# Performance work log

Measured on AMD Instinct MI355X. Metric: run time of the kernel, lower is better.

The kernel has to match this reference:

```python
import math
import jax, jax.numpy as jnp
import numpy as np

KV_RANK = 512
NOPE = 128
ROPE = 64
V_DIM = 128
N_HEADS = 16
DIM = 2048
EPS = 1e-6
# qk_head_dim = 192; max_seq_len > original_seq_len -> mscale correction
_MSCALE = 0.1 * 1.0 * math.log(40.0) + 1.0
SOFTMAX_SCALE = (NOPE + ROPE) ** -0.5 * _MSCALE * _MSCALE


def _rmsnorm(x, w):
    y = x * jax.lax.rsqrt(jnp.mean(x * x, axis=-1, keepdims=True) + EPS)
    return y * w


def _rope(x, cos, sin):
    # x: [b, s, h, d] with d even; pairs are interleaved (complex view semantics)
    xr, xi = x[..., 0::2], x[..., 1::2]
    c = cos[None, :, None, :]
    s = sin[None, :, None, :]
    yr = xr * c - xi * s
    yi = xr * s + xi * c
    return jnp.stack([yr, yi], axis=-1).reshape(x.shape)


def setup_inputs() -> dict:
    key = jax.random.key(0)
    ks = jax.random.split(key, 6)
    B, S = 2, 2048
    x = jax.random.normal(ks[0], (B, S, DIM), dtype=jnp.float32)
    # standard RoPE angles: pos * inv_freq, theta=10000
    inv_freq = 1.0 / (10000.0 ** (np.arange(0, ROPE, 2, dtype=np.float32) / ROPE))
    angles = jnp.asarray(np.arange(S, dtype=np.float32)[:, None] * inv_freq[None, :])
    wq = jax.random.normal(ks[1], (N_HEADS * (NOPE + ROPE), DIM), dtype=jnp.float32) * (DIM ** -0.5)
    wkv_a = jax.random.normal(ks[2], (KV_RANK + ROPE, DIM), dtype=jnp.float32) * (DIM ** -0.5)
    wkv_b = jax.random.normal(ks[3], (N_HEADS * (NOPE + V_DIM), KV_RANK), dtype=jnp.float32) * (KV_RANK ** -0.5)
    wo = jax.random.normal(ks[4], (DIM, N_HEADS * V_DIM), dtype=jnp.float32) * ((N_HEADS * V_DIM) ** -0.5)
    kv_norm_w = jnp.ones((KV_RANK,), dtype=jnp.float32)
    return {"x": x, "angles": angles, "wq": wq, "wkv_a": wkv_a,
            "wkv_b": wkv_b, "wo": wo, "kv_norm_w": kv_norm_w}


def reference(x, angles, wq, wkv_a, wkv_b, wo, kv_norm_w):
    B, S, _ = x.shape
    cos, sin = jnp.cos(angles), jnp.sin(angles)  # [S, ROPE//2]

    # query projection
    q = (x @ wq.T).reshape(B, S, N_HEADS, NOPE + ROPE)
    q_nope, q_pe = q[..., :NOPE], q[..., NOPE:]
    q_pe = _rope(q_pe, cos, sin)

    # low-rank kv projection
    kv = x @ wkv_a.T  # [B, S, KV_RANK + ROPE]
    kv_c, k_pe = kv[..., :KV_RANK], kv[..., KV_RANK:]
    k_pe = _rope(k_pe[:, :, None, :], cos, sin)[:, :, 0]  # [B, S, ROPE]
    c = _rmsnorm(kv_c, kv_norm_w)  # latent kv cache [B, S, KV_RANK]

    # weight absorption: fold W^UK into q
    wkv_b_h = wkv_b.reshape(N_HEADS, NOPE + V_DIM, KV_RANK)
    q_abs = jnp.einsum('bshd,hdc->bshc', q_nope, wkv_b_h[:, :NOPE])

    scores = (jnp.einsum('bshc,btc->bsht', q_abs, c)
              + jnp.einsum('bshr,btr->bsht', q_pe, k_pe)) * SOFTMAX_SCALE

    # causal mask (prefill, start_pos=0)
    mask = jnp.where(jnp.tril(jnp.ones((S, S), dtype=bool)), 0.0, -jnp.inf)
    scores = scores + mask[None, :, None, :]
    probs = jax.nn.softmax(scores.astype(jnp.float32), axis=-1).astype(x.dtype)

    o_lat = jnp.einsum('bsht,btc->bshc', probs, c)
    o = jnp.einsum('bshc,hdc->bshd', o_lat, wkv_b_h[:, NOPE:])  # [B,S,H,V]
    return o.reshape(B, S, N_HEADS * V_DIM) @ wo.T
```

## Files before the change

### kernel.cpp

```cpp
#include <hip/hip_runtime.h>
#include <hip/hip_bf16.h>

typedef unsigned short u16;
typedef unsigned int   u32;
typedef __attribute__((ext_vector_type(8))) short bf16x8;
typedef __attribute__((ext_vector_type(4))) float f32x4;

#define NH   16
#define SS   2048

__device__ __forceinline__ u16 bf16b(float f) {
  union { float f; u32 u; } v; v.f = f;
  u32 r = (v.u + 0x7fffu + ((v.u >> 16) & 1u)) >> 16;
  return (u16)r;
}
__device__ __forceinline__ float bf2f(u16 v) {
  union { u32 u; float f; } x; x.u = (u32)v << 16; return x.f;
}
__device__ __forceinline__ f32x4 mfma16(bf16x8 a, bf16x8 b, f32x4 c) {
  return __builtin_amdgcn_mfma_f32_16x16x32_bf16(a, b, c, 0, 0, 0);
}
__device__ __forceinline__ void gl_lds16(const u16* g, u16* l) {
  __builtin_amdgcn_global_load_lds(
      (const __attribute__((address_space(1))) void*)g,
      (__attribute__((address_space(3))) void*)l, 16, 0, 0);
}

__global__ __launch_bounds__(256) void zerok(float* __restrict__ p, long n)
{
  long i = ((long)blockIdx.x * 256 + threadIdx.x) * 4;
  if (i < n) { p[i] = 0.f; p[i+1] = 0.f; p[i+2] = 0.f; p[i+3] = 0.f; }
}

__global__ __launch_bounds__(256) void castk(const float* __restrict__ src,
                                             u16* __restrict__ dst, long n)
{
  long i = ((long)blockIdx.x * 256 + threadIdx.x) * 4;
  if (i >= n) return;
  const float4 f = *(const float4*)(src + i);
  uint2 v;
  v.x = (u32)bf16b(f.x) | ((u32)bf16b(f.y) << 16);
  v.y = (u32)bf16b(f.z) | ((u32)bf16b(f.w) << 16);
  *(uint2*)(dst + i) = v;
}

__global__ __launch_bounds__(256) void wsplit(const float* __restrict__ wb,
                                              u16* __restrict__ T1, u16* __restrict__ Wv)
{
  const long i = (long)blockIdx.x * 256 + threadIdx.x;
  const int h   = (int)(i >> 16);
  const int rem = (int)(i & 65535);
  { const int c = rem >> 7, d = rem & 127;
    T1[i] = bf16b(wb[((long)(h * 256 + d)) * 512 + c]); }
  { const int d = rem >> 9, c = rem & 511;
    Wv[i] = bf16b(wb[((long)(h * 256 + 128 + d)) * 512 + c]); }
}

template<int OUTBF>
__global__ __launch_bounds__(256, 2)
void gemm_bt(const u16* __restrict__ A, const u16* __restrict__ W, void* __restrict__ Cout,
             int M, int N, int K, int lda, int ldw, int ldc,
             long aStride, long wStride, long cStride)
{
  __shared__ u16 As[128 * 40];
  __shared__ u16 Bs[128 * 40];
  const int tid = threadIdx.x;
  const int wave = tid >> 6, lane = tid & 63, g = lane >> 4, l15 = lane & 15;
  const int z = blockIdx.z;
  A += (long)z * aStride;  W += (long)z * wStride;
  const long cOff = (long)z * cStride;
  const int m0 = blockIdx.y * 128, n0 = blockIdx.x * 128;
  const int mq = (wave >> 1) * 64, nq = (wave & 1) * 64;
  const int srow = tid >> 1, scol = (tid & 1) * 16;

  const f32x4 fzero = {0.f, 0.f, 0.f, 0.f};
  f32x4 acc[4][4];
#pragma unroll
  for (int i = 0; i < 4; i++)
#pragma unroll
    for (int j = 0; j < 4; j++) acc[i][j] = fzero;

  for (int k0 = 0; k0 < K; k0 += 32) {
    const u16* aSrc = A + (long)(m0 + srow) * lda + k0 + scol;
    uint4 av0 = *(const uint4*)aSrc;
    uint4 av1 = *(const uint4*)(aSrc + 8);
    uint4 bv0 = make_uint4(0, 0, 0, 0), bv1 = make_uint4(0, 0, 0, 0);
    if (n0 + srow < N) {
      const u16* wSrc = W + (long)(n0 + srow) * ldw + k0 + scol;
      bv0 = *(const uint4*)wSrc;
      bv1 = *(const uint4*)(wSrc + 8);
    }
    __syncthreads();
    *(uint4*)&As[srow * 40 + scol]     = av0;
    *(uint4*)&As[srow * 40 + scol + 8] = av1;
    *(uint4*)&Bs[srow * 40 + scol]     = bv0;
    *(uint4*)&Bs[srow * 40 + scol + 8] = bv1;
    __syncthreads();

    bf16x8 af[4], bfr[4];
#pragma unroll
    for (int i = 0; i < 4; i++) af[i]  = *(const bf16x8*)&As[(mq + i * 16 + l15) * 40 + g * 8];
#pragma unroll
    for (int j = 0; j < 4; j++) bfr[j] = *(const bf16x8*)&Bs[(nq + j * 16 + l15) * 40 + g * 8];
#pragma unroll
    for (int i = 0; i < 4; i++)
#pragma unroll
      for (int j = 0; j < 4; j++)
        acc[i][j] = mfma16(af[i], bfr[j], acc[i][j]);
  }

#pragma unroll
  for (int i = 0; i < 4; i++) {
    const int r0 = m0 + mq + i * 16 + g * 4;
#pragma unroll
    for (int j = 0; j < 4; j++) {
      const int c = n0 + nq + j * 16 + l15;
      if (c < N) {
#pragma unroll
        for (int r = 0; r < 4; r++) {
          const long idx = cOff + (long)(r0 + r) * ldc + c;
          if (OUTBF) ((u16*)Cout)[idx]   = bf16b(acc[i][j][r]);
          else       ((float*)Cout)[idx] = acc[i][j][r];
        }
      }
    }
  }
}

__global__ __launch_bounds__(256) void qpack(const u16* __restrict__ q,
                                             const float* __restrict__ angles,
                                             u16* __restrict__ qpe)
{
  const int s = blockIdx.x;
  const int sseq = s & (SS - 1);
  const int tid = threadIdx.x;
#pragma unroll
  for (int pp = 0; pp < 2; pp++) {
    const int p = tid * 2 + pp;
    const int h = p >> 5, j = p & 31;
    const float xr = bf2f(q[(long)s * 3072 + h * 192 + 128 + 2 * j]);
    const float xi = bf2f(q[(long)s * 3072 + h * 192 + 128 + 2 * j + 1]);
    float sn, cs;
    __sincosf(angles[sseq * 32 + j], &sn, &cs);
    const u32 pk = (u32)bf16b(xr * cs - xi * sn) | ((u32)bf16b(xr * sn + xi * cs) << 16);
    *(u32*)(qpe + ((long)s * NH + h) * 64 + 2 * j) = pk;
  }
}

__global__ __launch_bounds__(256) void kvpack(const u16* __restrict__ kv,
                                              const float* __restrict__ angles,
                                              const float* __restrict__ kvw,
                                              u16* __restrict__ cb, u16* __restrict__ kpe)
{
  const int row = blockIdx.x * 4 + (threadIdx.x >> 6);
  const int lane = threadIdx.x & 63;
  const int sseq = row & (SS - 1);
  const u16* src = kv + (long)row * 576;
  float v[8]; float ss = 0.f;
#pragma unroll
  for (int j = 0; j < 8; j++) { float t = bf2f(src[lane + j * 64]); v[j] = t; ss += t * t; }
#pragma unroll
  for (int d = 1; d < 64; d <<= 1) ss += __shfl_xor(ss, d, 64);
  const float rn = 1.0f / sqrtf(ss * (1.f / 512.f) + 1e-6f);
#pragma unroll
  for (int j = 0; j < 8; j++)
    cb[(long)row * 512 + lane + j * 64] = bf16b(v[j] * rn * kvw[lane + j * 64]);
  if (lane < 32) {
    const float xr = bf2f(src[512 + 2 * lane]), xi = bf2f(src[512 + 2 * lane + 1]);
    float sn, cs;
    __sincosf(angles[sseq * 32 + lane], &sn, &cs);
    const u32 pk = (u32)bf16b(xr * cs - xi * sn) | ((u32)bf16b(xr * sn + xi * cs) << 16);
    *(u32*)(kpe + (long)row * 64 + 2 * lane) = pk;
  }
}

__global__ __launch_bounds__(256, 2)
void attn_flash(const u16* __restrict__ qab, const u16* __restrict__ qpe,
                const u16* __restrict__ cb, const u16* __restrict__ kpe,
                u16* __restrict__ olat)
{
  __shared__ u16 KsD[2][16 * 512];
  __shared__ u16 KrD[2][16 * 64];
  __shared__ u16 VT[512 * 32];
  __shared__ u16 Ps[4][16 * 40];

  const int tid = threadIdx.x;
  const int wave = tid >> 6, lane = tid & 63;
  const int g = lane >> 4, l15 = lane & 15;
  const int bh = blockIdx.y, b = bh >> 4, h = bh & 15;
  const int bx = blockIdx.x;
  const int s0 = bx * 64;
  const int swave = s0 + wave * 16;
  const float NEG_INF = -__builtin_inff();
  const float SC = 0.07216878364870323f * 1.3688879454113936f * 1.3688879454113936f;

  for (int idx = tid; idx < 4 * 16 * 40 / 2; idx += 256) ((u32*)Ps)[idx] = 0;
  for (int idx = tid; idx < 512 * 32 / 2;   idx += 256) ((u32*)VT)[idx] = 0;

  bf16x8 qf[18];
  {
    const u16* qa = qab + ((long)(b * SS + swave + l15) * NH + h) * 512;
#pragma unroll
    for (int f = 0; f < 16; f++) qf[f] = *(const bf16x8*)(qa + f * 32 + g * 8);
    const u16* qp = qpe + ((long)(b * SS + swave + l15) * NH + h) * 64;
    qf[16] = *(const bf16x8*)(qp + g * 8);
    qf[17] = *(const bf16x8*)(qp + 32 + g * 8);
  }

  const f32x4 fzero = {0.f, 0.f, 0.f, 0.f};
  f32x4 oacc[32];
#pragma unroll
  for (int i = 0; i < 32; i++) oacc[i] = fzero;
  float m[4], l[4];
#pragma unroll
  for (int r = 0; r < 4; r++) { m[r] = NEG_INF; l[r] = 0.f; }

  const int nsteps  = 4 * bx + 4;
  const int lastact = 4 * bx + wave;

  const int tp   = tid & 7;
  const int cblk = tid >> 3;

  auto stage = [&](int t0n, int buf) {
#pragma unroll
    for (int it = 0; it < 4; ++it) {
      const int tr = it * 4 + wave;
      const int sw = ((tr >> 1) & 7) << 3;
      const u16* gp = cb + (long)(b * SS + t0n + tr) * 512 + ((lane * 8) ^ sw);
      gl_lds16(gp, &KsD[buf][tr * 512]);
    }
    if (wave < 2) {
      const int r0 = wave * 8;
      const int tr = r0 + (lane >> 3);
      const int sw = ((tr >> 1) & 7) << 3;
      const u16* gp = kpe + (long)(b * SS + t0n + tr) * 64 + (((lane & 7) * 8) ^ sw);
      gl_lds16(gp, &KrD[buf][r0 * 64]);
    }
  };

  stage(0, 0);

  for (int ts = 0; ts < nsteps; ++ts) {
    const int cur = ts & 1;
    const int t0 = ts * 16;
    asm volatile("s_waitcnt vmcnt(0) lgkmcnt(0)" ::: "memory");
    __builtin_amdgcn_s_barrier();

    if (ts + 1 < nsteps) stage(t0 + 16, cur ^ 1);

    {
      const u16* K0 = &KsD[cur][(2 * tp) * 512];
      const u16* K1 = &KsD[cur][(2 * tp + 1) * 512];
      const int swr  = (tp & 7) << 3;
      const int cb16 = cblk * 16;
      const bf16x8 alo = *(const bf16x8*)&K0[(cb16)     ^ swr];
      const bf16x8 ahi = *(const bf16x8*)&K0[(cb16 + 8) ^ swr];
      const bf16x8 blo = *(const bf16x8*)&K1[(cb16)     ^ swr];
      const bf16x8 bhi = *(const bf16x8*)&K1[(cb16 + 8) ^ swr];
#pragma unroll
      for (int j = 0; j < 16; ++j) {
        const int c = cb16 + j;
        const u16 ua = (u16)((j < 8) ? alo[j] : ahi[j - 8]);
        const u16 ub = (u16)((j < 8) ? blo[j] : bhi[j - 8]);
        *(u32*)&VT[(c * 32 + 2 * tp) ^ ((cblk & 7) << 3)] = (u32)ua | ((u32)ub << 16);
      }
    }
    asm volatile("s_waitcnt lgkmcnt(0)" ::: "memory");
    __builtin_amdgcn_s_barrier();

    if (ts > lastact) continue;

    const int swl = ((l15 >> 1) & 7) << 3;
    const u16* KsC = &KsD[cur][l15 * 512];
    const u16* KrC = &KrD[cur][l15 * 64];
    f32x4 sacc = fzero, sacc2 = fzero;
#pragma unroll
    for (int f = 0; f < 16; f += 2) {
      const bf16x8 k0 = *(const bf16x8*)&KsC[((f    ) * 32 + g * 8) ^ swl];
      const bf16x8 k1 = *(const bf16x8*)&KsC[((f + 1) * 32 + g * 8) ^ swl];
      sacc  = mfma16(qf[f],     k0, sacc);
      sacc2 = mfma16(qf[f + 1], k1, sacc2);
    }
    {
      const bf16x8 k0 = *(const bf16x8*)&KrC[(     g * 8) ^ swl];
      const bf16x8 k1 = *(const bf16x8*)&KrC[(32 + g * 8) ^ swl];
      sacc  = mfma16(qf[16], k0, sacc);
      sacc2 = mfma16(qf[17], k1, sacc2);
    }

    float alf[4]; bool resc = false;
#pragma unroll
    for (int r = 0; r < 4; ++r) {
      const int srow = swave + g * 4 + r;
      float v = (sacc[r] + sacc2[r]) * SC;
      if (t0 + l15 > srow) v = NEG_INF;
      float tm = v;
#pragma unroll
      for (int d = 1; d < 16; d <<= 1) tm = fmaxf(tm, __shfl_xor(tm, d, 64));
      const float mnew = (tm > m[r] + 8.f) ? tm : m[r];
      const float al = __expf(m[r] - mnew);
      const float p  = __expf(v - mnew);
      float rs = p;
#pragma unroll
      for (int d = 1; d < 16; d <<= 1) rs += __shfl_xor(rs, d, 64);
      l[r] = l[r] * al + rs;
      resc |= (mnew != m[r]);
      m[r] = mnew;
      alf[r] = al;
      Ps[wave][(g * 4 + r) * 40 + l15] = bf16b(p);
    }

    if (__any((int)resc)) {
#pragma unroll
      for (int i = 0; i < 32; ++i) {
        f32x4 o = oacc[i];
        o[0] *= alf[0]; o[1] *= alf[1]; o[2] *= alf[2]; o[3] *= alf[3];
        oacc[i] = o;
      }
    }

    const bf16x8 paf = *(const bf16x8*)&Ps[wave][l15 * 40 + g * 8];
#pragma unroll
    for (int i = 0; i < 32; ++i) {
      const int c = i * 16 + l15;
      const bf16x8 vf = *(const bf16x8*)&VT[(c * 32 + g * 8) ^ ((i & 7) << 3)];
      oacc[i] = mfma16(paf, vf, oacc[i]);
    }
  }

  float linv[4];
#pragma unroll
  for (int r = 0; r < 4; ++r) linv[r] = 1.0f / l[r];
#pragma unroll
  for (int r = 0; r < 4; ++r) {
    u16* dst = olat + ((long)(b * SS + swave + g * 4 + r) * NH + h) * 512 + l15;
#pragma unroll
    for (int i = 0; i < 32; ++i)
      dst[i * 16] = bf16b(oacc[i][r] * linv[r]);
  }
}

extern "C" void kernel_launch(void* const* d_in, const int* in_sizes, int n_in,
                              void* d_out, int out_size, void* d_ws, size_t ws_size,
                              hipStream_t stream)
{
  const float* x      = (const float*)d_in[0];
  const float* angles = (const float*)d_in[1];
  const float* wq     = (const float*)d_in[2];
  const float* wkv_a  = (const float*)d_in[3];
  const float* wkv_b  = (const float*)d_in[4];
  const float* wo     = (const float*)d_in[5];
  const float* kvw    = (const float*)d_in[6];

  const size_t WS_NEED = 157810688;
  if (ws_size < WS_NEED) {
    zerok<<<dim3(8192), dim3(256), 0, stream>>>((float*)d_out, 8388608L);
    return;
  }
  char* base = (char*)d_ws;
  u16* xb   = (u16*)(base + 0);
  u16* kvb  = (u16*)(base + 16777216);
  u16* wab  = (u16*)(base + 21495808);
  u16* qab  = (u16*)(base + 0);
  u16* ob   = (u16*)(base + 0);
  u16* qbf  = (u16*)(base + 67108864);
  u16* T1   = (u16*)(base + 92274688);
  u16* wqb  = (u16*)(base + 94371840);
  u16* olat = (u16*)(base + 67108864);
  u16* wob  = (u16*)(base + 134217728);
  u16* Wv   = (u16*)(base + 142606336);
  u16* qpe_ = (u16*)(base + 144703488);
  u16* cbuf = (u16*)(base + 153092096);
  u16* kpeb = (u16*)(base + 157286400);

  castk<<<dim3(8192), dim3(256), 0, stream>>>(x, xb, 8388608L);
  castk<<<dim3(6144), dim3(256), 0, stream>>>(wq, wqb, 6291456L);
  castk<<<dim3(1152), dim3(256), 0, stream>>>(wkv_a, wab, 1179648L);
  castk<<<dim3(4096), dim3(256), 0, stream>>>(wo, wob, 4194304L);
  wsplit<<<dim3(4096), dim3(256), 0, stream>>>(wkv_b, T1, Wv);

  gemm_bt<1><<<dim3(24, 32, 1), dim3(256), 0, stream>>>(
      xb, wqb, (void*)qbf, 4096, 3072, 2048, 2048, 2048, 3072, 0L, 0L, 0L);
  gemm_bt<1><<<dim3(5, 32, 1), dim3(256), 0, stream>>>(
      xb, wab, (void*)kvb, 4096, 576, 2048, 2048, 2048, 576, 0L, 0L, 0L);

  qpack<<<dim3(4096), dim3(256), 0, stream>>>(qbf, angles, qpe_);
  kvpack<<<dim3(1024), dim3(256), 0, stream>>>(kvb, angles, kvw, cbuf, kpeb);

  gemm_bt<1><<<dim3(4, 32, 16), dim3(256), 0, stream>>>(
      qbf, T1, (void*)qab, 4096, 512, 128, 3072, 128, 8192, 192L, 65536L, 512L);

  attn_flash<<<dim3(32, 32), dim3(256), 0, stream>>>(qab, qpe_, cbuf, kpeb, olat);

  gemm_bt<1><<<dim3(1, 32, 16), dim3(256), 0, stream>>>(
      olat, Wv, (void*)ob, 4096, 128, 512, 8192, 512, 2048, 512L, 65536L, 128L);

  gemm_bt<0><<<dim3(16, 32, 1), dim3(256), 0, stream>>>(
      ob, wob, d_out, 4096, 2048, 2048, 2048, 2048, 2048, 0L, 0L, 0L);
}
```

Measured before the change: 1.691 ms.

## Pair causal query tiles per block and use K16 MFMA for PV

```diff
diff --git a/kernel.cpp b/kernel.cpp
--- a/kernel.cpp
+++ b/kernel.cpp
@@ -4,6 +4,7 @@
 typedef unsigned short u16;
 typedef unsigned int   u32;
 typedef __attribute__((ext_vector_type(8))) short bf16x8;
+typedef __attribute__((ext_vector_type(4))) short bf16x4;
 typedef __attribute__((ext_vector_type(4))) float f32x4;
 
 #define NH   16
@@ -19,6 +20,16 @@
 }
 __device__ __forceinline__ f32x4 mfma16(bf16x8 a, bf16x8 b, f32x4 c) {
   return __builtin_amdgcn_mfma_f32_16x16x32_bf16(a, b, c, 0, 0, 0);
+}
+__device__ __forceinline__ f32x4 mfma16k16(bf16x4 a, bf16x4 b, f32x4 c) {
+#if __has_builtin(__builtin_amdgcn_mfma_f32_16x16x16bf16_1k)
+  return __builtin_amdgcn_mfma_f32_16x16x16bf16_1k(a, b, c, 0, 0, 0);
+#else
+  f32x4 d;
+  asm volatile("v_mfma_f32_16x16x16_bf16 %0, %1, %2, %3"
+               : "=v"(d) : "v"(a), "v"(b), "v"(c));
+  return d;
+#endif
 }
 __device__ __forceinline__ void gl_lds16(const u16* g, u16* l) {
   __builtin_amdgcn_global_load_lds(
@@ -181,42 +192,17 @@
 {
   __shared__ u16 KsD[2][16 * 512];
   __shared__ u16 KrD[2][16 * 64];
-  __shared__ u16 VT[512 * 32];
-  __shared__ u16 Ps[4][16 * 40];
+  __shared__ u16 VT16[512 * 16];
+  __shared__ u16 Ps[4][16 * 20];
 
   const int tid = threadIdx.x;
   const int wave = tid >> 6, lane = tid & 63;
   const int g = lane >> 4, l15 = lane & 15;
   const int bh = blockIdx.y, b = bh >> 4, h = bh & 15;
-  const int bx = blockIdx.x;
-  const int s0 = bx * 64;
-  const int swave = s0 + wave * 16;
+  const int pair = blockIdx.x;
   const float NEG_INF = -__builtin_inff();
   const float SC = 0.07216878364870323f * 1.3688879454113936f * 1.3688879454113936f;
-
-  for (int idx = tid; idx < 4 * 16 * 40 / 2; idx += 256) ((u32*)Ps)[idx] = 0;
-  for (int idx = tid; idx < 512 * 32 / 2;   idx += 256) ((u32*)VT)[idx] = 0;
-
-  bf16x8 qf[18];
-  {
-    const u16* qa = qab + ((long)(b * SS + swave + l15) * NH + h) * 512;
-#pragma unroll
-    for (int f = 0; f < 16; f++) qf[f] = *(const bf16x8*)(qa + f * 32 + g * 8);
-    const u16* qp = qpe + ((long)(b * SS + swave + l15) * NH + h) * 64;
-    qf[16] = *(const bf16x8*)(qp + g * 8);
-    qf[17] = *(const bf16x8*)(qp + 32 + g * 8);
-  }
-
   const f32x4 fzero = {0.f, 0.f, 0.f, 0.f};
-  f32x4 oacc[32];
-#pragma unroll
-  for (int i = 0; i < 32; i++) oacc[i] = fzero;
-  float m[4], l[4];
-#pragma unroll
-  for (int r = 0; r < 4; r++) { m[r] = NEG_INF; l[r] = 0.f; }
-
-  const int nsteps  = 4 * bx + 4;
-  const int lastact = 4 * bx + wave;
 
   const int tp   = tid & 7;
   const int cblk = tid >> 3;
@@ -238,105 +224,139 @@
     }
   };
 
-  stage(0, 0);
-
-  for (int ts = 0; ts < nsteps; ++ts) {
-    const int cur = ts & 1;
-    const int t0 = ts * 16;
-    asm volatile("s_waitcnt vmcnt(0) lgkmcnt(0)" ::: "memory");
-    __builtin_amdgcn_s_barrier();
-
-    if (ts + 1 < nsteps) stage(t0 + 16, cur ^ 1);
-
+#pragma unroll 1
+  for (int half = 0; half < 2; ++half) {
+    const int qt = half ? pair : (31 - pair);
+    const int swave = qt * 64 + wave * 16;
+
+    bf16x8 qf[18];
     {
-      const u16* K0 = &KsD[cur][(2 * tp) * 512];
-      const u16* K1 = &KsD[cur][(2 * tp + 1) * 512];
-      const int swr  = (tp & 7) << 3;
-      const int cb16 = cblk * 16;
-      const bf16x8 alo = *(const bf16x8*)&K0[(cb16)     ^ swr];
-      const bf16x8 ahi = *(const bf16x8*)&K0[(cb16 + 8) ^ swr];
-      const bf16x8 blo = *(const bf16x8*)&K1[(cb16)     ^ swr];
-      const bf16x8 bhi = *(const bf16x8*)&K1[(cb16 + 8) ^ swr];
-#pragma unroll
-      for (int j = 0; j < 16; ++j) {
-        const int c = cb16 + j;
-        const u16 ua = (u16)((j < 8) ? alo[j] : ahi[j - 8]);
-        const u16 ub = (u16)((j < 8) ? blo[j] : bhi[j - 8]);
-        *(u32*)&VT[(c * 32 + 2 * tp) ^ ((cblk & 7) << 3)] = (u32)ua | ((u32)ub << 16);
+      const u16* qa = qab + ((long)(b * SS + swave + l15) * NH + h) * 512;
+#pragma unroll
+      for (int f = 0; f < 16; f++) qf[f] = *(const bf16x8*)(qa + f * 32 + g * 8);
+      const u16* qp = qpe + ((long)(b * SS + swave + l15) * NH + h) * 64;
+      qf[16] = *(const bf16x8*)(qp + g * 8);
+      qf[17] = *(const bf16x8*)(qp + 32 + g * 8);
+    }
+
+    f32x4 oacc[32];
+#pragma unroll
+    for (int i = 0; i < 32; i++) oacc[i] = fzero;
+    float m[4], l[4];
+#pragma unroll
+    for (int r = 0; r < 4; r++) { m[r] = NEG_INF; l[r] = 0.f; }
+
+    const int nsteps  = 4 * qt + 4;
+    const int lastact = 4 * qt + wave;
+
+    stage(0, 0);
+
+    for (int ts = 0; ts < nsteps; ++ts) {
+      const int cur = ts & 1;
+      const int t0 = ts * 16;
+      asm volatile("s_waitcnt vmcnt(0) lgkmcnt(0)" ::: "memory");
+      __builtin_amdgcn_s_barrier();
+
+      if (ts + 1 < nsteps) stage(t0 + 16, cur ^ 1);
+
+      {
+        const u16* K0 = &KsD[cur][(2 * tp) * 512];
+        const u16* K1 = &KsD[cur][(2 * tp + 1) * 512];
+        const int swr  = (tp & 7) << 3;
+        const int cb16 = cblk * 16;
+        const bf16x8 alo = *(const bf16x8*)&K0[(cb16)     ^ swr];
+        const bf16x8 ahi = *(const bf16x8*)&K0[(cb16 + 8) ^ swr];
+        const bf16x8 blo = *(const bf16x8*)&K1[(cb16)     ^ swr];
+        const bf16x8 bhi = *(const bf16x8*)&K1[(cb16 + 8) ^ swr];
+#pragma unroll
+        for (int j = 0; j < 16; ++j) {
+          const int c = cb16 + j;
+          const u16 ua = (u16)((j < 8) ? alo[j] : ahi[j - 8]);
+          const u16 ub = (u16)((j < 8) ? blo[j] : bhi[j - 8]);
+          *(u32*)&VT16[(c * 16 + 2 * tp) ^ ((cblk & 7) << 3)] = (u32)ua | ((u32)ub << 16);
+        }
       }
-    }
-    asm volatile("s_waitcnt lgkmcnt(0)" ::: "memory");
-    __builtin_amdgcn_s_barrier();
-
-    if (ts > lastact) continue;
-
-    const int swl = ((l15 >> 1) & 7) << 3;
-    const u16* KsC = &KsD[cur][l15 * 512];
-    const u16* KrC = &KrD[cur][l15 * 64];
-    f32x4 sacc = fzero, sacc2 = fzero;
-#pragma unroll
-    for (int f = 0; f < 16; f += 2) {
-      const bf16x8 k0 = *(const bf16x8*)&KsC[((f    ) * 32 + g * 8) ^ swl];
-      const bf16x8 k1 = *(const bf16x8*)&KsC[((f + 1) * 32 + g * 8) ^ swl];
-      sacc  = mfma16(qf[f],     k0, sacc);
-      sacc2 = mfma16(qf[f + 1], k1, sacc2);
-    }
-    {
-      const bf16x8 k0 = *(const bf16x8*)&KrC[(     g * 8) ^ swl];
-      const bf16x8 k1 = *(const bf16x8*)&KrC[(32 + g * 8) ^ swl];
-      sacc  = mfma16(qf[16], k0, sacc);
-      sacc2 = mfma16(qf[17], k1, sacc2);
-    }
-
-    float alf[4]; bool resc = false;
+
+      const bool active = (ts <= lastact);
+      float alf[4]; bool resc = false;
+      if (active) {
+        const int swl = ((l15 >> 1) & 7) << 3;
+        const u16* KsC = &KsD[cur][l15 * 512];
+        const u16* KrC = &KrD[cur][l15 * 64];
+        f32x4 sacc = fzero, sacc2 = fzero;
+        __builtin_amdgcn_s_setprio(1);
+#pragma unroll
+        for (int f = 0; f < 16; f += 2) {
+          const bf16x8 k0 = *(const bf16x8*)&KsC[((f    ) * 32 + g * 8) ^ swl];
+          const bf16x8 k1 = *(const bf16x8*)&KsC[((f + 1) * 32 + g * 8) ^ swl];
+          sacc  = mfma16(qf[f],     k0, sacc);
+          sacc2 = mfma16(qf[f + 1], k1, sacc2);
+        }
+        {
+          const bf16x8 k0 = *(const bf16x8*)&KrC[(     g * 8) ^ swl];
+          const bf16x8 k1 = *(const bf16x8*)&KrC[(32 + g * 8) ^ swl];
+          sacc  = mfma16(qf[16], k0, sacc);
+          sacc2 = mfma16(qf[17], k1, sacc2);
+        }
+        __builtin_amdgcn_s_setprio(0);
+
+#pragma unroll
+        for (int r = 0; r < 4; ++r) {
+          const int srow = swave + g * 4 + r;
+          float v = (sacc[r] + sacc2[r]) * SC;
+          if (t0 + l15 > srow) v = NEG_INF;
+          float tm = v;
+#pragma unroll
+          for (int d = 1; d < 16; d <<= 1) tm = fmaxf(tm, __shfl_xor(tm, d, 64));
+          const float mnew = (tm > m[r] + 8.f) ? tm : m[r];
+          const float al = __expf(m[r] - mnew);
+          const float p  = __expf(v - mnew);
+          float rs = p;
+#pragma unroll
+          for (int d = 1; d < 16; d <<= 1) rs += __shfl_xor(rs, d, 64);
+          l[r] = l[r] * al + rs;
+          resc |= (mnew != m[r]);
+          m[r] = mnew;
+          alf[r] = al;
+          Ps[wave][(g * 4 + r) * 20 + l15] = bf16b(p);
+        }
+
+        if (__any((int)resc)) {
+#pragma unroll
+          for (int i = 0; i < 32; ++i) {
+            f32x4 o = oacc[i];
+            o[0] *= alf[0]; o[1] *= alf[1]; o[2] *= alf[2]; o[3] *= alf[3];
+            oacc[i] = o;
+          }
+        }
+      }
+
+      asm volatile("s_waitcnt lgkmcnt(0)" ::: "memory");
+      __builtin_amdgcn_s_barrier();
+
+      if (active) {
+        const bf16x4 paf = *(const bf16x4*)&Ps[wave][l15 * 20 + g * 4];
+        __builtin_amdgcn_s_setprio(1);
+#pragma unroll
+        for (int i = 0; i < 32; ++i) {
+          const int c = i * 16 + l15;
+          const bf16x4 vf = *(const bf16x4*)&VT16[(c * 16 + g * 4) ^ ((i & 7) << 3)];
+          oacc[i] = mfma16k16(paf, vf, oacc[i]);
+        }
+        __builtin_amdgcn_s_setprio(0);
+      }
+    }
+
+    float linv[4];
+#pragma unroll
+    for (int r = 0; r < 4; ++r) linv[r] = 1.0f / l[r];
 #pragma unroll
     for (int r = 0; r < 4; ++r) {
-      const int srow = swave + g * 4 + r;
-      float v = (sacc[r] + sacc2[r]) * SC;
-      if (t0 + l15 > srow) v = NEG_INF;
-      float tm = v;
-#pragma unroll
-      for (int d = 1; d < 16; d <<= 1) tm = fmaxf(tm, __shfl_xor(tm, d, 64));
-      const float mnew = (tm > m[r] + 8.f) ? tm : m[r];
-      const float al = __expf(m[r] - mnew);
-      const float p  = __expf(v - mnew);
-      float rs = p;
-#pragma unroll
-      for (int d = 1; d < 16; d <<= 1) rs += __shfl_xor(rs, d, 64);
-      l[r] = l[r] * al + rs;
-      resc |= (mnew != m[r]);
-      m[r] = mnew;
-      alf[r] = al;
-      Ps[wave][(g * 4 + r) * 40 + l15] = bf16b(p);
-    }
-
-    if (__any((int)resc)) {
-#pragma unroll
-      for (int i = 0; i < 32; ++i) {
-        f32x4 o = oacc[i];
-        o[0] *= alf[0]; o[1] *= alf[1]; o[2] *= alf[2]; o[3] *= alf[3];
-        oacc[i] = o;
-      }
-    }
-
-    const bf16x8 paf = *(const bf16x8*)&Ps[wave][l15 * 40 + g * 8];
-#pragma unroll
-    for (int i = 0; i < 32; ++i) {
-      const int c = i * 16 + l15;
-      const bf16x8 vf = *(const bf16x8*)&VT[(c * 32 + g * 8) ^ ((i & 7) << 3)];
-      oacc[i] = mfma16(paf, vf, oacc[i]);
-    }
-  }
-
-  float linv[4];
-#pragma unroll
-  for (int r = 0; r < 4; ++r) linv[r] = 1.0f / l[r];
-#pragma unroll
-  for (int r = 0; r < 4; ++r) {
-    u16* dst = olat + ((long)(b * SS + swave + g * 4 + r) * NH + h) * 512 + l15;
-#pragma unroll
-    for (int i = 0; i < 32; ++i)
-      dst[i * 16] = bf16b(oacc[i][r] * linv[r]);
+      u16* dst = olat + ((long)(b * SS + swave + g * 4 + r) * NH + h) * 512 + l15;
+#pragma unroll
+      for (int i = 0; i < 32; ++i)
+        dst[i * 16] = bf16b(oacc[i][r] * linv[r]);
+    }
   }
 }
 
@@ -390,7 +410,7 @@
   gemm_bt<1><<<dim3(4, 32, 16), dim3(256), 0, stream>>>(
       qbf, T1, (void*)qab, 4096, 512, 128, 3072, 128, 8192, 192L, 65536L, 512L);
 
-  attn_flash<<<dim3(32, 32), dim3(256), 0, stream>>>(qab, qpe_, cbuf, kpeb, olat);
+  attn_flash<<<dim3(16, 32), dim3(256), 0, stream>>>(qab, qpe_, cbuf, kpeb, olat);
 
   gemm_bt<1><<<dim3(1, 32, 16), dim3(256), 0, stream>>>(
       olat, Wv, (void*)ob, 4096, 128, 512, 8192, 512, 2048, 512L, 65536L, 128L);
```

Result: slower. 1.852 ms (+9.5%).
